# Kernel tuning notes

Hardware: AMD Instinct MI355X
Metric: run time of the kernel (lower is better)

The kernel has to match this reference:

```python
import jax, jax.numpy as jnp
import numpy as np
from jax import lax

B, C_IN, H, W = 16, 2048, 16, 16
HIDDEN, N_ANC = 512, 9
N_POS, N_NEG = 2048, 2048
TOT = B * N_ANC * H * W  # 36864 = flat conf logits; also rows of reg.view(-1,4)


def _xyxy_to_cxcywh(b):
    x1, y1, x2, y2 = b[..., 0], b[..., 1], b[..., 2], b[..., 3]
    return jnp.stack([(x1 + x2) * 0.5, (y1 + y2) * 0.5, x2 - x1, y2 - y1], axis=-1)


def _cxcywh_to_xyxy(b):
    cx, cy, w, h = b[..., 0], b[..., 1], b[..., 2], b[..., 3]
    return jnp.stack([cx - w * 0.5, cy - h * 0.5, cx + w * 0.5, cy + h * 0.5], axis=-1)


def _rand_boxes(key, n):
    # valid xyxy boxes on the 16x16 feature-map coordinate grid, w,h in [1,4]
    k1, k2 = jax.random.split(key)
    xy = jax.random.uniform(k1, (n, 2), jnp.float32) * 12.0
    wh = 1.0 + jax.random.uniform(k2, (n, 2), jnp.float32) * 3.0
    return jnp.concatenate([xy, xy + wh], axis=-1)


def setup_inputs() -> dict:
    key = jax.random.key(0)
    ks = jax.random.split(key, 10)
    feature_map = jax.random.normal(ks[0], (B, C_IN, H, W), jnp.float32)
    pos_anc_ind = jax.random.randint(ks[1], (N_POS,), 0, TOT)
    neg_anc_ind = jax.random.randint(ks[2], (N_NEG,), 0, TOT)
    pos_anc_coords = _rand_boxes(ks[3], N_POS)
    gt_bboxes_pos = _rand_boxes(ks[4], N_POS)
    s1 = 1.0 / np.sqrt(C_IN * 9)
    W1 = jax.random.uniform(ks[5], (HIDDEN, C_IN, 3, 3), jnp.float32, -s1, s1)
    b1 = jnp.zeros((HIDDEN,), jnp.float32)
    s2 = 1.0 / np.sqrt(HIDDEN)
    Wc = jax.random.uniform(ks[6], (N_ANC, HIDDEN), jnp.float32, -s2, s2)
    bc = jnp.zeros((N_ANC,), jnp.float32)
    Wr = jax.random.uniform(ks[7], (N_ANC * 4, HIDDEN), jnp.float32, -s2, s2)
    br = jnp.zeros((N_ANC * 4,), jnp.float32)
    return {"feature_map": feature_map, "pos_anc_coords": pos_anc_coords,
            "gt_bboxes_pos": gt_bboxes_pos, "W1": W1, "b1": b1, "Wc": Wc,
            "bc": bc, "Wr": Wr, "br": br,
            "pos_anc_ind": pos_anc_ind, "neg_anc_ind": neg_anc_ind}


def generate_proposals(anchors, offsets):
    a = _xyxy_to_cxcywh(anchors)
    p = jnp.stack([a[:, 0] + offsets[:, 0] * a[:, 2],
                   a[:, 1] + offsets[:, 1] * a[:, 3],
                   a[:, 2] * jnp.exp(offsets[:, 2]),
                   a[:, 3] * jnp.exp(offsets[:, 3])], axis=-1)
    return _cxcywh_to_xyxy(p)


def calc_gt_offsets(anc, gt):
    a = _xyxy_to_cxcywh(anc)
    g = _xyxy_to_cxcywh(gt)
    tx = (g[:, 0] - a[:, 0]) / a[:, 2]
    ty = (g[:, 1] - a[:, 1]) / a[:, 3]
    tw = jnp.log(g[:, 2] / a[:, 2])
    th = jnp.log(g[:, 3] / a[:, 3])
    return jnp.stack([tx, ty, tw, th], axis=-1)


def reference(feature_map, pos_anc_coords, gt_bboxes_pos, W1, b1, Wc, bc, Wr, br,
              pos_anc_ind, neg_anc_ind):
    # ProposalModule: conv3x3 -> (dropout=identity in eval) -> relu -> 1x1 heads
    out = lax.conv_general_dilated(feature_map, W1, (1, 1), 'SAME',
                                   dimension_numbers=('NCHW', 'OIHW', 'NCHW'))
    out = jax.nn.relu(out + b1[None, :, None, None])
    conf = jnp.einsum('bchw,oc->bohw', out, Wc) + bc[None, :, None, None]   # [B,9,H,W]
    reg = jnp.einsum('bchw,oc->bohw', out, Wr) + br[None, :, None, None]    # [B,36,H,W]
    # irregular flat gathers, exactly mirroring torch .flatten()/.view(-1,4)
    conf_pos = conf.reshape(-1)[pos_anc_ind]
    conf_neg = conf.reshape(-1)[neg_anc_ind]
    offsets_pos = reg.reshape(-1, 4)[pos_anc_ind]
    proposals = generate_proposals(pos_anc_coords, offsets_pos)
    gt_offsets = calc_gt_offsets(pos_anc_coords, gt_bboxes_pos)
    # BCE-with-logits, targets 1 for pos / 0 for neg, reduction='sum' / B
    cls_loss = (jnp.sum(jax.nn.softplus(-conf_pos)) + jnp.sum(jax.nn.softplus(conf_neg))) / B
    # smooth L1 (beta=1), reduction='sum' / B
    d = offsets_pos - gt_offsets
    ad = jnp.abs(d)
    reg_loss = jnp.sum(jnp.where(ad < 1.0, 0.5 * d * d, ad - 0.5)) / B
    total_rpn_loss = 1.0 * cls_loss + 5.0 * reg_loss  # w_conf=1, w_reg=5
    return total_rpn_loss, proposals
```

## Files before the change

### kernel.cpp

```cpp
#include <hip/hip_runtime.h>
#include <hip/hip_bf16.h>
#include <stdint.h>

#define CIN 2048
#define HID 512
#define NPOS 2048
#define NNEG 2048

#define BM 256
#define BN 256
#define BK 64
#define A_ELEMS (BM * BK)
#define B_ELEMS (BN * BK)

typedef __attribute__((ext_vector_type(8))) short s16x8;
typedef __attribute__((ext_vector_type(4))) short s16x4;
typedef __attribute__((ext_vector_type(4))) float f32x4;
typedef unsigned short ushort_t;

static __device__ __forceinline__ unsigned short f2bf(float f) {
    union { float f; unsigned int i; } v; v.f = f;
    unsigned int r = v.i + 0x7FFF + ((v.i >> 16) & 1);
    return (unsigned short)(r >> 16);
}

typedef __attribute__((address_space(1))) const void gvoid_t;
typedef __attribute__((address_space(3))) void lvoid_t;
static __device__ __forceinline__ void gload16(const void* g, void* l) {
    __builtin_amdgcn_global_load_lds((gvoid_t*)g, (lvoid_t*)l, 16, 0, 0);
}

__global__ __launch_bounds__(256) void k_prep(const float* __restrict__ F,
                                              const float* __restrict__ W1,
                                              ushort_t* __restrict__ Fp,
                                              ushort_t* __restrict__ Wt2) {
    __shared__ float tile[64][17];
    __shared__ float buf[512 * 9];
    int bid = blockIdx.x;
    int t = threadIdx.x;
    if (bid < 256) {
        int b = bid >> 4, y = bid & 15;
        for (int ic0 = 0; ic0 < CIN; ic0 += 64) {
            {
                int ci = t >> 2, xg = t & 3;
                const float4 v = *(const float4*)&F[((size_t)(b * CIN + ic0 + ci) * 16 + y) * 16 + xg * 4];
                tile[ci][xg * 4 + 0] = v.x;
                tile[ci][xg * 4 + 1] = v.y;
                tile[ci][xg * 4 + 2] = v.z;
                tile[ci][xg * 4 + 3] = v.w;
            }
            __syncthreads();
            {
                int x = t >> 4, cig = t & 15;
                s16x4 o;
#pragma unroll
                for (int j = 0; j < 4; ++j) o[j] = (short)f2bf(tile[cig * 4 + j][x]);
                *(s16x4*)&Fp[((size_t)(b * 18 + y + 1) * 18 + (x + 1)) * CIN + ic0 + cig * 4] = o;
            }
            __syncthreads();
        }
    } else if (bid < 768) {
        int oc = bid - 256;
        for (int ic0 = 0; ic0 < CIN; ic0 += 512) {
            const float* src = W1 + ((size_t)oc * CIN + ic0) * 9;
            for (int i = t; i < 512 * 9; i += 256) buf[i] = src[i];
            __syncthreads();
            for (int s = t; s < 9 * 64; s += 256) {
                int k = s >> 6, g = s & 63;
                s16x8 v;
#pragma unroll
                for (int j = 0; j < 8; ++j) v[j] = (short)f2bf(buf[(g * 8 + j) * 9 + k]);
                *(s16x8*)&Wt2[((size_t)(k * HID + oc)) * CIN + ic0 + g * 8] = v;
            }
            __syncthreads();
        }
    } else {
        const s16x8 z = {0, 0, 0, 0, 0, 0, 0, 0};
        for (int idx = (bid - 768) * 256 + t; idx < 16 * 68 * 256; idx += 64 * 256) {
            int seg = idx & 255;
            int cell = (idx >> 8) % 68;
            int b = idx / (68 * 256);
            int Y, X;
            if (cell < 18)      { Y = 0;         X = cell; }
            else if (cell < 36) { Y = 17;        X = cell - 18; }
            else if (cell < 52) { Y = cell - 35; X = 0; }
            else                { Y = cell - 51; X = 17; }
            *(s16x8*)&Fp[((size_t)(b * 18 + Y) * 18 + X) * CIN + seg * 8] = z;
        }
    }
}

__global__ __launch_bounds__(512, 2) void k_gemm(const ushort_t* __restrict__ Fp,
                                                 const ushort_t* __restrict__ Wt2,
                                                 float* __restrict__ Part,
                                                 int icLen, int nPairs) {
    extern __shared__ ushort_t ldsbuf[];
    ushort_t* As = ldsbuf;
    ushort_t* Bs = ldsbuf + 2 * A_ELEMS;

    int bid = blockIdx.x;
    int rb = bid / nPairs;
    int pair = bid - rb * nPairs;
    int split = pair >> 1, cb = pair & 1;
    int icBase = split * icLen;
    int m0 = rb * BM, oc0 = cb * BN;
    int t = threadIdx.x;
    int wid = t >> 6, lane = t & 63;
    int wr = wid >> 2, wn = wid & 3;
    int hi = lane >> 4, lo = lane & 15;

    f32x4 acc[8][4];
#pragma unroll
    for (int a = 0; a < 8; ++a)
#pragma unroll
        for (int b = 0; b < 4; ++b) acc[a][b] = (f32x4){0.f, 0.f, 0.f, 0.f};

    int Abase[4], Bbase[4];
#pragma unroll
    for (int j = 0; j < 4; ++j) {
        int li = j * 512 + t;
        int row = li >> 3;
        int sg = (li & 7) ^ (row & 7);
        int m = m0 + row;
        int b = m >> 8, y = (m >> 4) & 15, x = m & 15;
        Abase[j] = ((b * 18 + y) * 18 + x) * CIN + sg * 8;
        Bbase[j] = (oc0 + row) * CIN + sg * 8;
    }
    int aidx[8][2], bidx[4][2];
#pragma unroll
    for (int fm = 0; fm < 8; ++fm)
#pragma unroll
        for (int ks = 0; ks < 2; ++ks) {
            int r = wr * 128 + fm * 16 + lo;
            aidx[fm][ks] = r * BK + ((ks * 32 + hi * 8) ^ ((r & 7) << 3));
        }
#pragma unroll
    for (int fn = 0; fn < 4; ++fn)
#pragma unroll
        for (int ks = 0; ks < 2; ++ks) {
            int rB = wn * 64 + fn * 16 + lo;
            bidx[fn][ks] = rB * BK + ((ks * 32 + hi * 8) ^ ((rB & 7) << 3));
        }

    const int nsteps = (icLen / BK) * 9;

#define STAGE(BUF, S)                                                                \
    do {                                                                             \
        int kidx_ = (S) % 9, icc_ = (S) / 9;                                         \
        int ak_ = ((kidx_ / 3) * 18 + (kidx_ - 3 * (kidx_ / 3))) * CIN + icBase + icc_ * BK; \
        int bk_ = kidx_ * HID * CIN + icBase + icc_ * BK;                            \
        ushort_t* dA_ = As + (BUF) * A_ELEMS;                                        \
        ushort_t* dB_ = Bs + (BUF) * B_ELEMS;                                        \
        _Pragma("unroll") for (int j_ = 0; j_ < 4; ++j_) {                           \
            gload16(Fp + Abase[j_] + ak_, dA_ + (size_t)(j_ * 512 + t) * 8);         \
            gload16(Wt2 + Bbase[j_] + bk_, dB_ + (size_t)(j_ * 512 + t) * 8);        \
        }                                                                            \
    } while (0)

    STAGE(0, 0);
    asm volatile("s_waitcnt vmcnt(0)" ::: "memory");
    __builtin_amdgcn_s_barrier();
    __builtin_amdgcn_sched_barrier(0);

    int cur = 0;
#pragma unroll 1
    for (int step = 0; step < nsteps; ++step) {
        const ushort_t* cA = As + cur * A_ELEMS;
        const ushort_t* cB = Bs + cur * B_ELEMS;
        if (step + 1 < nsteps) STAGE(cur ^ 1, step + 1);
        s16x8 af[8][2], bf[4][2];
#pragma unroll
        for (int ks = 0; ks < 2; ++ks) {
#pragma unroll
            for (int fm = 0; fm < 8; ++fm) af[fm][ks] = *(const s16x8*)&cA[aidx[fm][ks]];
#pragma unroll
            for (int fn = 0; fn < 4; ++fn) bf[fn][ks] = *(const s16x8*)&cB[bidx[fn][ks]];
        }
        __builtin_amdgcn_s_setprio(1);
#pragma unroll
        for (int fm = 0; fm < 8; ++fm)
#pragma unroll
            for (int fn = 0; fn < 4; ++fn)
#pragma unroll
                for (int ks = 0; ks < 2; ++ks)
                    acc[fm][fn] = __builtin_amdgcn_mfma_f32_16x16x32_bf16(
                        af[fm][ks], bf[fn][ks], acc[fm][fn], 0, 0, 0);
        __builtin_amdgcn_s_setprio(0);
        if (step + 1 < nsteps) {
            asm volatile("s_waitcnt vmcnt(0)" ::: "memory");
            __builtin_amdgcn_s_barrier();
            __builtin_amdgcn_sched_barrier(0);
        }
        cur ^= 1;
    }
#undef STAGE

#pragma unroll
    for (int fm = 0; fm < 8; ++fm)
#pragma unroll
        for (int fn = 0; fn < 4; ++fn)
#pragma unroll
            for (int r = 0; r < 4; ++r) {
                int gm = m0 + wr * 128 + fm * 16 + hi * 4 + r;
                int gn = oc0 + wn * 64 + fn * 16 + lo;
                Part[((size_t)split * 4096 + gm) * HID + gn] = acc[fm][fn][r];
            }
}

__global__ __launch_bounds__(256) void k_heads(const float* __restrict__ Part, int ns,
                                               const float* __restrict__ b1,
                                               const float* __restrict__ Wc,
                                               const float* __restrict__ bc,
                                               const float* __restrict__ Wr,
                                               const float* __restrict__ br,
                                               float* __restrict__ conf,
                                               float* __restrict__ reg) {
    extern __shared__ ushort_t hsm[];
    ushort_t* Ah = hsm;
    ushort_t* Wh = hsm + 16 * HID;
    int t = threadIdx.x;
    int wid = t >> 6, lane = t & 63;
    int hi = lane >> 4, lo = lane & 15;
    int row0 = blockIdx.x * 16;

#pragma unroll
    for (int i = 0; i < 8; ++i) {
        int pos = i * 256 + t;
        int r = pos >> 7, c4 = (pos & 127) * 4;
        float4 s = {0.f, 0.f, 0.f, 0.f};
        for (int sp = 0; sp < ns; ++sp) {
            const float4 v = *(const float4*)&Part[((size_t)sp * 4096 + row0 + r) * HID + c4];
            s.x += v.x; s.y += v.y; s.z += v.z; s.w += v.w;
        }
        s.x = fmaxf(s.x + b1[c4 + 0], 0.f);
        s.y = fmaxf(s.y + b1[c4 + 1], 0.f);
        s.z = fmaxf(s.z + b1[c4 + 2], 0.f);
        s.w = fmaxf(s.w + b1[c4 + 3], 0.f);
        s16x4 o = {(short)f2bf(s.x), (short)f2bf(s.y), (short)f2bf(s.z), (short)f2bf(s.w)};
        int phys = r * HID + ((((c4 >> 3) ^ (r & 7)) << 3) | (c4 & 7));
        *(s16x4*)&Ah[phys] = o;
    }
#pragma unroll
    for (int i = 0; i < 12; ++i) {
        int sid = i * 256 + t;
        int o = sid >> 6, sg = sid & 63;
        s16x8 v;
#pragma unroll
        for (int j = 0; j < 8; ++j) {
            float w = 0.f;
            if (o < 9) w = Wc[o * HID + sg * 8 + j];
            else if (o < 45) w = Wr[(size_t)(o - 9) * HID + sg * 8 + j];
            v[j] = (short)f2bf(w);
        }
        *(s16x8*)&Wh[o * HID + ((sg ^ (o & 7)) << 3)] = v;
    }
    __syncthreads();
    if (wid != 0) return;

    f32x4 acc[3];
#pragma unroll
    for (int fn = 0; fn < 3; ++fn) acc[fn] = (f32x4){0.f, 0.f, 0.f, 0.f};
#pragma unroll 1
    for (int kf = 0; kf < 16; ++kf) {
        int rA = lo;
        s16x8 a_ = *(const s16x8*)&Ah[rA * HID + ((kf * 32 + hi * 8) ^ ((rA & 7) << 3))];
#pragma unroll
        for (int fn = 0; fn < 3; ++fn) {
            int rB = fn * 16 + lo;
            s16x8 b_ = *(const s16x8*)&Wh[rB * HID + ((kf * 32 + hi * 8) ^ ((rB & 7) << 3))];
            acc[fn] = __builtin_amdgcn_mfma_f32_16x16x32_bf16(a_, b_, acc[fn], 0, 0, 0);
        }
    }
#pragma unroll
    for (int fn = 0; fn < 3; ++fn)
#pragma unroll
        for (int r = 0; r < 4; ++r) {
            int gm = row0 + hi * 4 + r;
            int o = fn * 16 + lo;
            float v = acc[fn][r];
            if (o < 9) conf[gm * 9 + o] = v + bc[o];
            else if (o < 45) reg[gm * 36 + (o - 9)] = v + br[o - 9];
        }
}

static __device__ __forceinline__ float softplus(float x) {
    return log1pf(expf(-fabsf(x))) + fmaxf(x, 0.f);
}

__global__ __launch_bounds__(1024) void k_loss(const float* __restrict__ conf,
                                               const float* __restrict__ reg,
                                               const int* __restrict__ pos_ind,
                                               const int* __restrict__ neg_ind,
                                               const float* __restrict__ anc,
                                               const float* __restrict__ gt,
                                               float* __restrict__ out) {
    int t = threadIdx.x;
    float cls = 0.f, rloss = 0.f;
    for (int p = t; p < NPOS; p += 1024) {
        int ind = pos_ind[p];
        {
            int b = ind / 2304, r = ind % 2304;
            int c = r >> 8, r2 = r & 255;
            float cv = conf[(b * 256 + r2) * 9 + c];
            cls += softplus(-cv);
        }
        float off[4];
#pragma unroll
        for (int j = 0; j < 4; ++j) {
            int e = 4 * ind + j;
            int b = e / 9216, r = e % 9216;
            int c = r >> 8, r2 = r & 255;
            off[j] = reg[(b * 256 + r2) * 36 + c];
        }
        float ax1 = anc[4 * p], ay1 = anc[4 * p + 1], ax2 = anc[4 * p + 2], ay2 = anc[4 * p + 3];
        float acx = (ax1 + ax2) * 0.5f, acy = (ay1 + ay2) * 0.5f;
        float aw = ax2 - ax1, ah = ay2 - ay1;
        float pcx = acx + off[0] * aw, pcy = acy + off[1] * ah;
        float pw = aw * expf(off[2]), ph = ah * expf(off[3]);
        out[1 + 4 * p + 0] = pcx - pw * 0.5f;
        out[1 + 4 * p + 1] = pcy - ph * 0.5f;
        out[1 + 4 * p + 2] = pcx + pw * 0.5f;
        out[1 + 4 * p + 3] = pcy + ph * 0.5f;
        float gx1 = gt[4 * p], gy1 = gt[4 * p + 1], gx2 = gt[4 * p + 2], gy2 = gt[4 * p + 3];
        float gcx = (gx1 + gx2) * 0.5f, gcy = (gy1 + gy2) * 0.5f;
        float gw = gx2 - gx1, gh = gy2 - gy1;
        float tv[4];
        tv[0] = (gcx - acx) / aw;
        tv[1] = (gcy - acy) / ah;
        tv[2] = logf(gw / aw);
        tv[3] = logf(gh / ah);
#pragma unroll
        for (int j = 0; j < 4; ++j) {
            float d = off[j] - tv[j];
            float ad = fabsf(d);
            rloss += (ad < 1.f) ? 0.5f * d * d : ad - 0.5f;
        }
    }
    for (int q = t; q < NNEG; q += 1024) {
        int ind = neg_ind[q];
        int b = ind / 2304, r = ind % 2304;
        int c = r >> 8, r2 = r & 255;
        float cv = conf[(b * 256 + r2) * 9 + c];
        cls += softplus(cv);
    }
    __shared__ float s1[1024], s2[1024];
    s1[t] = cls;
    s2[t] = rloss;
    __syncthreads();
    for (int s = 512; s > 0; s >>= 1) {
        if (t < s) {
            s1[t] += s1[t + s];
            s2[t] += s2[t + s];
        }
        __syncthreads();
    }
    if (t == 0) out[0] = (s1[0] + 5.f * s2[0]) / 16.f;
}

extern "C" void kernel_launch(void* const* d_in, const int* in_sizes, int n_in,
                              void* d_out, int out_size, void* d_ws, size_t ws_size,
                              hipStream_t stream) {
    const float* F   = (const float*)d_in[0];
    const float* anc = (const float*)d_in[1];
    const float* gt  = (const float*)d_in[2];
    const float* W1  = (const float*)d_in[3];
    const float* b1  = (const float*)d_in[4];
    const float* Wc  = (const float*)d_in[5];
    const float* bc  = (const float*)d_in[6];
    const float* Wr  = (const float*)d_in[7];
    const float* br  = (const float*)d_in[8];
    const int* pos_ind = (const int*)d_in[9];
    const int* neg_ind = (const int*)d_in[10];
    float* out = (float*)d_out;

    char* ws = (char*)d_ws;
    const size_t FP_BYTES   = (size_t)16 * 18 * 18 * CIN * 2;
    const size_t WT_BYTES   = (size_t)9 * HID * CIN * 2;
    const size_t PART_ONE   = (size_t)4096 * HID * 4;
    const size_t CONF_BYTES = (size_t)4096 * 9 * 4;
    const size_t REG_BYTES  = (size_t)4096 * 36 * 4;

    int NS = 8;
    while (NS > 1 &&
           FP_BYTES + WT_BYTES + (size_t)NS * PART_ONE + CONF_BYTES + REG_BYTES > ws_size)
        NS >>= 1;
    int icLen = CIN / NS;

    ushort_t* Fp  = (ushort_t*)ws;
    ushort_t* Wt2 = (ushort_t*)(ws + FP_BYTES);
    float* Part   = (float*)(ws + FP_BYTES + WT_BYTES);
    float* conf   = (float*)(ws + FP_BYTES + WT_BYTES + (size_t)NS * PART_ONE);
    float* reg    = (float*)(ws + FP_BYTES + WT_BYTES + (size_t)NS * PART_ONE + CONF_BYTES);

    const int GEMM_LDS = 2 * (A_ELEMS + B_ELEMS) * 2;
    hipFuncSetAttribute((const void*)k_gemm, hipFuncAttributeMaxDynamicSharedMemorySize, GEMM_LDS);
    const int HEADS_LDS = (16 + 48) * HID * 2;
    hipFuncSetAttribute((const void*)k_heads, hipFuncAttributeMaxDynamicSharedMemorySize, HEADS_LDS);

    k_prep<<<832, 256, 0, stream>>>(F, W1, Fp, Wt2);
    k_gemm<<<(4096 / BM) * (HID / BN) * NS, 512, GEMM_LDS, stream>>>(Fp, Wt2, Part, icLen, 2 * NS);
    k_heads<<<256, 256, HEADS_LDS, stream>>>(Part, NS, b1, Wc, bc, Wr, br, conf, reg);
    k_loss<<<1, 1024, 0, stream>>>(conf, reg, pos_ind, neg_ind, anc, gt, out);
}
```

Before: 138.6 us.

## Use 4-stage BK=32 GEMM pipeline and bf16 split-K partials

The conv GEMM now stages K in chunks of 32 through a 4-deep LDS ring, prefetching three steps ahead and waiting with partial vmcnt, instead of double-buffered BK=64 chunks. The LDS swizzle and addressing are reworked to match. Split-K partial sums are stored as bf16 rather than fp32, halving partial-buffer traffic, and the heads kernel reads them with 16-byte loads. NS is fixed at 8 with no workspace-size fallback. The bf16 partials lose accuracy, and the smaller K step doubles the number of barriers per tile.

```diff
diff --git a/kernel.cpp b/kernel.cpp
--- a/kernel.cpp
+++ b/kernel.cpp
@@ -9,7 +9,8 @@
 
 #define BM 256
 #define BN 256
-#define BK 64
+#define BK 32
+#define NS 8
 #define A_ELEMS (BM * BK)
 #define B_ELEMS (BN * BK)
 
@@ -18,6 +19,9 @@
 typedef __attribute__((ext_vector_type(4))) float f32x4;
 typedef unsigned short ushort_t;
 
+static __device__ __forceinline__ float bf2f(unsigned short u) {
+    union { float f; unsigned int i; } v; v.i = ((unsigned int)u) << 16; return v.f;
+}
 static __device__ __forceinline__ unsigned short f2bf(float f) {
     union { float f; unsigned int i; } v; v.f = f;
     unsigned int r = v.i + 0x7FFF + ((v.i >> 16) & 1);
@@ -92,11 +96,11 @@
 
 __global__ __launch_bounds__(512, 2) void k_gemm(const ushort_t* __restrict__ Fp,
                                                  const ushort_t* __restrict__ Wt2,
-                                                 float* __restrict__ Part,
+                                                 ushort_t* __restrict__ Part,
                                                  int icLen, int nPairs) {
     extern __shared__ ushort_t ldsbuf[];
     ushort_t* As = ldsbuf;
-    ushort_t* Bs = ldsbuf + 2 * A_ELEMS;
+    ushort_t* Bs = ldsbuf + 4 * A_ELEMS;
 
     int bid = blockIdx.x;
     int rb = bid / nPairs;
@@ -115,32 +119,28 @@
 #pragma unroll
         for (int b = 0; b < 4; ++b) acc[a][b] = (f32x4){0.f, 0.f, 0.f, 0.f};
 
-    int Abase[4], Bbase[4];
-#pragma unroll
-    for (int j = 0; j < 4; ++j) {
+    int Abase[2], Bbase[2];
+#pragma unroll
+    for (int j = 0; j < 2; ++j) {
         int li = j * 512 + t;
-        int row = li >> 3;
-        int sg = (li & 7) ^ (row & 7);
+        int row = li >> 2;
+        int sg = (li & 3) ^ ((row >> 1) & 3);
         int m = m0 + row;
         int b = m >> 8, y = (m >> 4) & 15, x = m & 15;
         Abase[j] = ((b * 18 + y) * 18 + x) * CIN + sg * 8;
         Bbase[j] = (oc0 + row) * CIN + sg * 8;
     }
-    int aidx[8][2], bidx[4][2];
-#pragma unroll
-    for (int fm = 0; fm < 8; ++fm)
-#pragma unroll
-        for (int ks = 0; ks < 2; ++ks) {
-            int r = wr * 128 + fm * 16 + lo;
-            aidx[fm][ks] = r * BK + ((ks * 32 + hi * 8) ^ ((r & 7) << 3));
-        }
-#pragma unroll
-    for (int fn = 0; fn < 4; ++fn)
-#pragma unroll
-        for (int ks = 0; ks < 2; ++ks) {
-            int rB = wn * 64 + fn * 16 + lo;
-            bidx[fn][ks] = rB * BK + ((ks * 32 + hi * 8) ^ ((rB & 7) << 3));
-        }
+    int aidx[8], bidx[4];
+#pragma unroll
+    for (int fm = 0; fm < 8; ++fm) {
+        int r = wr * 128 + fm * 16 + lo;
+        aidx[fm] = r * BK + ((hi ^ ((r >> 1) & 3)) << 3);
+    }
+#pragma unroll
+    for (int fn = 0; fn < 4; ++fn) {
+        int rB = wn * 64 + fn * 16 + lo;
+        bidx[fn] = rB * BK + ((hi ^ ((rB >> 1) & 3)) << 3);
+    }
 
     const int nsteps = (icLen / BK) * 9;
 
@@ -151,47 +151,44 @@
         int bk_ = kidx_ * HID * CIN + icBase + icc_ * BK;                            \
         ushort_t* dA_ = As + (BUF) * A_ELEMS;                                        \
         ushort_t* dB_ = Bs + (BUF) * B_ELEMS;                                        \
-        _Pragma("unroll") for (int j_ = 0; j_ < 4; ++j_) {                           \
+        _Pragma("unroll") for (int j_ = 0; j_ < 2; ++j_) {                           \
             gload16(Fp + Abase[j_] + ak_, dA_ + (size_t)(j_ * 512 + t) * 8);         \
             gload16(Wt2 + Bbase[j_] + bk_, dB_ + (size_t)(j_ * 512 + t) * 8);        \
         }                                                                            \
     } while (0)
 
-    STAGE(0, 0);
-    asm volatile("s_waitcnt vmcnt(0)" ::: "memory");
+    STAGE(0, 0); STAGE(1, 1); STAGE(2, 2);
+    asm volatile("s_waitcnt vmcnt(8)" ::: "memory");
     __builtin_amdgcn_s_barrier();
     __builtin_amdgcn_sched_barrier(0);
 
-    int cur = 0;
 #pragma unroll 1
     for (int step = 0; step < nsteps; ++step) {
-        const ushort_t* cA = As + cur * A_ELEMS;
-        const ushort_t* cB = Bs + cur * B_ELEMS;
-        if (step + 1 < nsteps) STAGE(cur ^ 1, step + 1);
-        s16x8 af[8][2], bf[4][2];
-#pragma unroll
-        for (int ks = 0; ks < 2; ++ks) {
-#pragma unroll
-            for (int fm = 0; fm < 8; ++fm) af[fm][ks] = *(const s16x8*)&cA[aidx[fm][ks]];
-#pragma unroll
-            for (int fn = 0; fn < 4; ++fn) bf[fn][ks] = *(const s16x8*)&cB[bidx[fn][ks]];
-        }
+        const ushort_t* cA = As + (step & 3) * A_ELEMS;
+        const ushort_t* cB = Bs + (step & 3) * B_ELEMS;
+        if (step + 3 < nsteps) STAGE((step + 3) & 3, step + 3);
+        s16x8 af[8], bf[4];
+#pragma unroll
+        for (int fm = 0; fm < 8; ++fm) af[fm] = *(const s16x8*)&cA[aidx[fm]];
+#pragma unroll
+        for (int fn = 0; fn < 4; ++fn) bf[fn] = *(const s16x8*)&cB[bidx[fn]];
         __builtin_amdgcn_s_setprio(1);
 #pragma unroll
         for (int fm = 0; fm < 8; ++fm)
 #pragma unroll
             for (int fn = 0; fn < 4; ++fn)
-#pragma unroll
-                for (int ks = 0; ks < 2; ++ks)
-                    acc[fm][fn] = __builtin_amdgcn_mfma_f32_16x16x32_bf16(
-                        af[fm][ks], bf[fn][ks], acc[fm][fn], 0, 0, 0);
+                acc[fm][fn] = __builtin_amdgcn_mfma_f32_16x16x32_bf16(
+                    af[fm], bf[fn], acc[fm][fn], 0, 0, 0);
         __builtin_amdgcn_s_setprio(0);
-        if (step + 1 < nsteps) {
+        if (step + 3 < nsteps) {
+            asm volatile("s_waitcnt vmcnt(8)" ::: "memory");
+            __builtin_amdgcn_s_barrier();
+            __builtin_amdgcn_sched_barrier(0);
+        } else if (step + 1 < nsteps) {
             asm volatile("s_waitcnt vmcnt(0)" ::: "memory");
             __builtin_amdgcn_s_barrier();
             __builtin_amdgcn_sched_barrier(0);
         }
-        cur ^= 1;
     }
 #undef STAGE
 
@@ -203,11 +200,11 @@
             for (int r = 0; r < 4; ++r) {
                 int gm = m0 + wr * 128 + fm * 16 + hi * 4 + r;
                 int gn = oc0 + wn * 64 + fn * 16 + lo;
-                Part[((size_t)split * 4096 + gm) * HID + gn] = acc[fm][fn][r];
+                Part[((size_t)split * 4096 + gm) * HID + gn] = f2bf(acc[fm][fn][r]);
             }
 }
 
-__global__ __launch_bounds__(256) void k_heads(const float* __restrict__ Part, int ns,
+__global__ __launch_bounds__(256) void k_heads(const ushort_t* __restrict__ Part, int ns,
                                                const float* __restrict__ b1,
                                                const float* __restrict__ Wc,
                                                const float* __restrict__ bc,
@@ -224,21 +221,21 @@
     int row0 = blockIdx.x * 16;
 
 #pragma unroll
-    for (int i = 0; i < 8; ++i) {
+    for (int i = 0; i < 4; ++i) {
         int pos = i * 256 + t;
-        int r = pos >> 7, c4 = (pos & 127) * 4;
-        float4 s = {0.f, 0.f, 0.f, 0.f};
+        int r = pos >> 6, sg = pos & 63;
+        float s[8];
+#pragma unroll
+        for (int j = 0; j < 8; ++j) s[j] = 0.f;
         for (int sp = 0; sp < ns; ++sp) {
-            const float4 v = *(const float4*)&Part[((size_t)sp * 4096 + row0 + r) * HID + c4];
-            s.x += v.x; s.y += v.y; s.z += v.z; s.w += v.w;
-        }
-        s.x = fmaxf(s.x + b1[c4 + 0], 0.f);
-        s.y = fmaxf(s.y + b1[c4 + 1], 0.f);
-        s.z = fmaxf(s.z + b1[c4 + 2], 0.f);
-        s.w = fmaxf(s.w + b1[c4 + 3], 0.f);
-        s16x4 o = {(short)f2bf(s.x), (short)f2bf(s.y), (short)f2bf(s.z), (short)f2bf(s.w)};
-        int phys = r * HID + ((((c4 >> 3) ^ (r & 7)) << 3) | (c4 & 7));
-        *(s16x4*)&Ah[phys] = o;
+            s16x8 v = *(const s16x8*)&Part[((size_t)sp * 4096 + row0 + r) * HID + sg * 8];
+#pragma unroll
+            for (int j = 0; j < 8; ++j) s[j] += bf2f((unsigned short)v[j]);
+        }
+        s16x8 o;
+#pragma unroll
+        for (int j = 0; j < 8; ++j) o[j] = (short)f2bf(fmaxf(s[j] + b1[sg * 8 + j], 0.f));
+        *(s16x8*)&Ah[r * HID + ((sg ^ (r & 7)) << 3)] = o;
     }
 #pragma unroll
     for (int i = 0; i < 12; ++i) {
@@ -376,23 +373,18 @@
     char* ws = (char*)d_ws;
     const size_t FP_BYTES   = (size_t)16 * 18 * 18 * CIN * 2;
     const size_t WT_BYTES   = (size_t)9 * HID * CIN * 2;
-    const size_t PART_ONE   = (size_t)4096 * HID * 4;
+    const size_t PART_ONE   = (size_t)4096 * HID * 2;
     const size_t CONF_BYTES = (size_t)4096 * 9 * 4;
-    const size_t REG_BYTES  = (size_t)4096 * 36 * 4;
-
-    int NS = 8;
-    while (NS > 1 &&
-           FP_BYTES + WT_BYTES + (size_t)NS * PART_ONE + CONF_BYTES + REG_BYTES > ws_size)
-        NS >>= 1;
+
     int icLen = CIN / NS;
 
-    ushort_t* Fp  = (ushort_t*)ws;
-    ushort_t* Wt2 = (ushort_t*)(ws + FP_BYTES);
-    float* Part   = (float*)(ws + FP_BYTES + WT_BYTES);
-    float* conf   = (float*)(ws + FP_BYTES + WT_BYTES + (size_t)NS * PART_ONE);
-    float* reg    = (float*)(ws + FP_BYTES + WT_BYTES + (size_t)NS * PART_ONE + CONF_BYTES);
-
-    const int GEMM_LDS = 2 * (A_ELEMS + B_ELEMS) * 2;
+    ushort_t* Fp   = (ushort_t*)ws;
+    ushort_t* Wt2  = (ushort_t*)(ws + FP_BYTES);
+    ushort_t* Part = (ushort_t*)(ws + FP_BYTES + WT_BYTES);
+    float* conf    = (float*)(ws + FP_BYTES + WT_BYTES + (size_t)NS * PART_ONE);
+    float* reg     = (float*)(ws + FP_BYTES + WT_BYTES + (size_t)NS * PART_ONE + CONF_BYTES);
+
+    const int GEMM_LDS = 4 * (A_ELEMS + B_ELEMS) * 2;
     hipFuncSetAttribute((const void*)k_gemm, hipFuncAttributeMaxDynamicSharedMemorySize, GEMM_LDS);
     const int HEADS_LDS = (16 + 48) * HID * 2;
     hipFuncSetAttribute((const void*)k_heads, hipFuncAttributeMaxDynamicSharedMemorySize, HEADS_LDS);
```

Result: faster. 134.5 us (-2.9%).

## Store split-K partials in bf16 and parallelize feature-map prep across more blocks

Applied to the files above, without the earlier changes.

The GEMM's split-K partial sums are now written as bf16 instead of fp32, which halves the partial buffer traffic written by k_gemm and read by k_heads. k_heads reads 8 bf16 values per load and accumulates them in fp32. k_prep splits the feature transpose over four times as many blocks (one per channel quarter) and copies weights with float4 loads. The split count is fixed at 8 instead of being chosen to fit the workspace, so the code now relies on the workspace being large enough, and rounding each partial to bf16 adds precision loss.

```diff
diff --git a/kernel.cpp b/kernel.cpp
--- a/kernel.cpp
+++ b/kernel.cpp
@@ -10,6 +10,7 @@
 #define BM 256
 #define BN 256
 #define BK 64
+#define NS 8
 #define A_ELEMS (BM * BK)
 #define B_ELEMS (BN * BK)
 
@@ -18,6 +19,9 @@
 typedef __attribute__((ext_vector_type(4))) float f32x4;
 typedef unsigned short ushort_t;
 
+static __device__ __forceinline__ float bf2f(unsigned short u) {
+    union { float f; unsigned int i; } v; v.i = ((unsigned int)u) << 16; return v.f;
+}
 static __device__ __forceinline__ unsigned short f2bf(float f) {
     union { float f; unsigned int i; } v; v.f = f;
     unsigned int r = v.i + 0x7FFF + ((v.i >> 16) & 1);
@@ -38,9 +42,11 @@
     __shared__ float buf[512 * 9];
     int bid = blockIdx.x;
     int t = threadIdx.x;
-    if (bid < 256) {
-        int b = bid >> 4, y = bid & 15;
-        for (int ic0 = 0; ic0 < CIN; ic0 += 64) {
+    if (bid < 1024) {
+        int b = bid >> 6, rem = bid & 63;
+        int y = rem >> 2, icq = rem & 3;
+        for (int i = 0; i < 8; ++i) {
+            int ic0 = icq * 512 + i * 64;
             {
                 int ci = t >> 2, xg = t & 3;
                 const float4 v = *(const float4*)&F[((size_t)(b * CIN + ic0 + ci) * 16 + y) * 16 + xg * 4];
@@ -59,11 +65,15 @@
             }
             __syncthreads();
         }
-    } else if (bid < 768) {
-        int oc = bid - 256;
+    } else if (bid < 1536) {
+        int oc = bid - 1024;
         for (int ic0 = 0; ic0 < CIN; ic0 += 512) {
             const float* src = W1 + ((size_t)oc * CIN + ic0) * 9;
-            for (int i = t; i < 512 * 9; i += 256) buf[i] = src[i];
+            {
+                const float4* s4 = (const float4*)src;
+                float4* b4 = (float4*)buf;
+                for (int i = t; i < 1152; i += 256) b4[i] = s4[i];
+            }
             __syncthreads();
             for (int s = t; s < 9 * 64; s += 256) {
                 int k = s >> 6, g = s & 63;
@@ -76,7 +86,7 @@
         }
     } else {
         const s16x8 z = {0, 0, 0, 0, 0, 0, 0, 0};
-        for (int idx = (bid - 768) * 256 + t; idx < 16 * 68 * 256; idx += 64 * 256) {
+        for (int idx = (bid - 1536) * 256 + t; idx < 16 * 68 * 256; idx += 64 * 256) {
             int seg = idx & 255;
             int cell = (idx >> 8) % 68;
             int b = idx / (68 * 256);
@@ -92,7 +102,7 @@
 
 __global__ __launch_bounds__(512, 2) void k_gemm(const ushort_t* __restrict__ Fp,
                                                  const ushort_t* __restrict__ Wt2,
-                                                 float* __restrict__ Part,
+                                                 ushort_t* __restrict__ Part,
                                                  int icLen, int nPairs) {
     extern __shared__ ushort_t ldsbuf[];
     ushort_t* As = ldsbuf;
@@ -203,11 +213,11 @@
             for (int r = 0; r < 4; ++r) {
                 int gm = m0 + wr * 128 + fm * 16 + hi * 4 + r;
                 int gn = oc0 + wn * 64 + fn * 16 + lo;
-                Part[((size_t)split * 4096 + gm) * HID + gn] = acc[fm][fn][r];
+                Part[((size_t)split * 4096 + gm) * HID + gn] = f2bf(acc[fm][fn][r]);
             }
 }
 
-__global__ __launch_bounds__(256) void k_heads(const float* __restrict__ Part, int ns,
+__global__ __launch_bounds__(256) void k_heads(const ushort_t* __restrict__ Part, int ns,
                                                const float* __restrict__ b1,
                                                const float* __restrict__ Wc,
                                                const float* __restrict__ bc,
@@ -224,21 +234,21 @@
     int row0 = blockIdx.x * 16;
 
 #pragma unroll
-    for (int i = 0; i < 8; ++i) {
+    for (int i = 0; i < 4; ++i) {
         int pos = i * 256 + t;
-        int r = pos >> 7, c4 = (pos & 127) * 4;
-        float4 s = {0.f, 0.f, 0.f, 0.f};
+        int r = pos >> 6, sg = pos & 63;
+        float s[8];
+#pragma unroll
+        for (int j = 0; j < 8; ++j) s[j] = 0.f;
         for (int sp = 0; sp < ns; ++sp) {
-            const float4 v = *(const float4*)&Part[((size_t)sp * 4096 + row0 + r) * HID + c4];
-            s.x += v.x; s.y += v.y; s.z += v.z; s.w += v.w;
-        }
-        s.x = fmaxf(s.x + b1[c4 + 0], 0.f);
-        s.y = fmaxf(s.y + b1[c4 + 1], 0.f);
-        s.z = fmaxf(s.z + b1[c4 + 2], 0.f);
-        s.w = fmaxf(s.w + b1[c4 + 3], 0.f);
-        s16x4 o = {(short)f2bf(s.x), (short)f2bf(s.y), (short)f2bf(s.z), (short)f2bf(s.w)};
-        int phys = r * HID + ((((c4 >> 3) ^ (r & 7)) << 3) | (c4 & 7));
-        *(s16x4*)&Ah[phys] = o;
+            s16x8 v = *(const s16x8*)&Part[((size_t)sp * 4096 + row0 + r) * HID + sg * 8];
+#pragma unroll
+            for (int j = 0; j < 8; ++j) s[j] += bf2f((unsigned short)v[j]);
+        }
+        s16x8 o;
+#pragma unroll
+        for (int j = 0; j < 8; ++j) o[j] = (short)f2bf(fmaxf(s[j] + b1[sg * 8 + j], 0.f));
+        *(s16x8*)&Ah[r * HID + ((sg ^ (r & 7)) << 3)] = o;
     }
 #pragma unroll
     for (int i = 0; i < 12; ++i) {
@@ -376,28 +386,23 @@
     char* ws = (char*)d_ws;
     const size_t FP_BYTES   = (size_t)16 * 18 * 18 * CIN * 2;
     const size_t WT_BYTES   = (size_t)9 * HID * CIN * 2;
-    const size_t PART_ONE   = (size_t)4096 * HID * 4;
+    const size_t PART_ONE   = (size_t)4096 * HID * 2;
     const size_t CONF_BYTES = (size_t)4096 * 9 * 4;
-    const size_t REG_BYTES  = (size_t)4096 * 36 * 4;
-
-    int NS = 8;
-    while (NS > 1 &&
-           FP_BYTES + WT_BYTES + (size_t)NS * PART_ONE + CONF_BYTES + REG_BYTES > ws_size)
-        NS >>= 1;
+
     int icLen = CIN / NS;
 
-    ushort_t* Fp  = (ushort_t*)ws;
-    ushort_t* Wt2 = (ushort_t*)(ws + FP_BYTES);
-    float* Part   = (float*)(ws + FP_BYTES + WT_BYTES);
-    float* conf   = (float*)(ws + FP_BYTES + WT_BYTES + (size_t)NS * PART_ONE);
-    float* reg    = (float*)(ws + FP_BYTES + WT_BYTES + (size_t)NS * PART_ONE + CONF_BYTES);
+    ushort_t* Fp   = (ushort_t*)ws;
+    ushort_t* Wt2  = (ushort_t*)(ws + FP_BYTES);
+    ushort_t* Part = (ushort_t*)(ws + FP_BYTES + WT_BYTES);
+    float* conf    = (float*)(ws + FP_BYTES + WT_BYTES + (size_t)NS * PART_ONE);
+    float* reg     = (float*)(ws + FP_BYTES + WT_BYTES + (size_t)NS * PART_ONE + CONF_BYTES);
 
     const int GEMM_LDS = 2 * (A_ELEMS + B_ELEMS) * 2;
     hipFuncSetAttribute((const void*)k_gemm, hipFuncAttributeMaxDynamicSharedMemorySize, GEMM_LDS);
     const int HEADS_LDS = (16 + 48) * HID * 2;
     hipFuncSetAttribute((const void*)k_heads, hipFuncAttributeMaxDynamicSharedMemorySize, HEADS_LDS);
 
-    k_prep<<<832, 256, 0, stream>>>(F, W1, Fp, Wt2);
+    k_prep<<<1600, 256, 0, stream>>>(F, W1, Fp, Wt2);
     k_gemm<<<(4096 / BM) * (HID / BN) * NS, 512, GEMM_LDS, stream>>>(Fp, Wt2, Part, icLen, 2 * NS);
     k_heads<<<256, 256, HEADS_LDS, stream>>>(Part, NS, b1, Wc, bc, Wr, br, conf, reg);
     k_loss<<<1, 1024, 0, stream>>>(conf, reg, pos_ind, neg_ind, anc, gt, out);
```

New measurement: 127.5 us. 1.09x faster.
